# Kernel optimization log

Hardware: AMD Instinct MI355X
Metric: run time of the kernel (lower is better)

Reference implementation:

```python
import jax, jax.numpy as jnp
import numpy as np

IN_CH = 256
INTER_CH = IN_CH // 2  # reduction=2


def setup_inputs() -> dict:
    key = jax.random.key(0)
    ks = jax.random.split(key, 9)
    x = jax.random.normal(ks[0], (8, IN_CH, 64, 64), dtype=jnp.float32)
    std = 0.01
    # 1x1 conv weights stored as [out_ch, in_ch] (kernel is 1x1)
    Wg = jax.random.normal(ks[1], (INTER_CH, IN_CH), dtype=jnp.float32) * std
    bg = jnp.zeros((INTER_CH,), dtype=jnp.float32)
    Wt = jax.random.normal(ks[2], (INTER_CH, IN_CH), dtype=jnp.float32) * std
    bt = jnp.zeros((INTER_CH,), dtype=jnp.float32)
    Wp = jax.random.normal(ks[3], (INTER_CH, IN_CH), dtype=jnp.float32) * std
    bp = jnp.zeros((INTER_CH,), dtype=jnp.float32)
    # conv_out is zero-initialized in the module; use small random values so
    Wo = jax.random.normal(ks[4], (IN_CH, INTER_CH), dtype=jnp.float32) * std
    bo = jnp.zeros((IN_CH,), dtype=jnp.float32)
    return {"x": x, "Wg": Wg, "bg": bg, "Wt": Wt, "bt": bt,
            "Wp": Wp, "bp": bp, "Wo": Wo, "bo": bo}


def reference(x, Wg, bg, Wt, bt, Wp, bp, Wo, bo):
    n, c, h, w = x.shape
    s = h * w
    xf = x.reshape(n, c, s)  # [n, C, S]
    # 1x1 conv projections (no downsample, embedded_gaussian mode)
    g_x = jnp.einsum('kc,ncs->nsk', Wg, xf) + bg          # [n, S, K]
    theta_x = jnp.einsum('kc,ncs->nsk', Wt, xf) + bt      # [n, S, K]
    phi_x = jnp.einsum('kc,ncs->nks', Wp, xf) + bp[:, None]  # [n, K, S]
    # embedded_gaussian: scores -> scale (fixbug: / sqrt(K)) -> /temp(=1) -> softmax
    scale = 1.0 / jnp.sqrt(jnp.asarray(INTER_CH, dtype=x.dtype))
    scores = jnp.einsum('nsk,nkt->nst', theta_x, phi_x) * scale  # [n, S, S]
    pw = jax.nn.softmax(scores, axis=-1)
    y = jnp.einsum('nst,ntk->nsk', pw, g_x)               # [n, S, K]
    out = xf + jnp.einsum('ck,nsk->ncs', Wo, y) + bo[None, :, None]
    return out.reshape(n, c, h, w)
```

## Files before the change

kernel.cpp:

```cpp
#include <hip/hip_runtime.h>
#include <hip/hip_bf16.h>

#define NB   8
#define CCH  256
#define KCH  128
#define SSP  4096

typedef unsigned short u16;
typedef __attribute__((ext_vector_type(8))) short  bfrag;
typedef __attribute__((ext_vector_type(4))) float  ffrag;

#define MFMA16(a, b, c) __builtin_amdgcn_mfma_f32_16x16x32_bf16((a), (b), (c), 0, 0, 0)
#define SWZ(i, r) ((unsigned)(i) ^ ((((unsigned)(r)) & 7u) << 3))

#define GLDS(G, L) __builtin_amdgcn_global_load_lds(                          \
    (const __attribute__((address_space(1))) void*)(G),                       \
    (__attribute__((address_space(3))) void*)(L), 16, 0, 0)

__device__ __forceinline__ u16 f2b(float f) {
    union { float f; unsigned u; } v; v.f = f;
    return (u16)((v.u + 0x7fffu + ((v.u >> 16) & 1u)) >> 16);
}

__global__ __launch_bounds__(256, 2) void proj_gp_kernel(
    const float* __restrict__ x,
    const float* __restrict__ Wg, const float* __restrict__ bg,
    const float* __restrict__ Wp, const float* __restrict__ bp,
    u16* __restrict__ G,
    u16* __restrict__ P)
{
    __shared__ __align__(16) u16 sm[25600];
    const int tid  = threadIdx.x;
    const int wv   = tid >> 6;
    const int lane = tid & 63;
    const int quad = lane >> 4, l16 = lane & 15;
    const int bid  = blockIdx.x;
    const int n  = bid & 7;
    const int s0 = (bid >> 3) * 64;

    const ffrag zf = {0.f, 0.f, 0.f, 0.f};
    ffrag ga[8], pa[8];
#pragma unroll
    for (int kb = 0; kb < 8; kb++) { ga[kb] = zf; pa[kb] = zf; }

    float4 xreg[2], wgreg[4], wpreg[4];

#define K1_LOAD(C0)                                                          \
    {                                                                        \
        _Pragma("unroll")                                                    \
        for (int i = 0; i < 2; i++) {                                        \
            int f = tid + i * 256;                                           \
            int c = f >> 4, s4 = (f & 15) * 4;                               \
            xreg[i] = *(const float4*)&x[((size_t)n * CCH + (C0) + c) * SSP + s0 + s4]; \
        }                                                                    \
        _Pragma("unroll")                                                    \
        for (int i = 0; i < 4; i++) {                                        \
            int f = tid + i * 256;                                           \
            int k = f >> 3, co = (f & 7) * 4;                                \
            wgreg[i] = *(const float4*)&Wg[k * CCH + (C0) + co];             \
            wpreg[i] = *(const float4*)&Wp[k * CCH + (C0) + co];             \
        }                                                                    \
    }

#define K1_COMMIT(B)                                                         \
    {                                                                        \
        const int bb = (B) * 12800;                                          \
        _Pragma("unroll")                                                    \
        for (int i = 0; i < 2; i++) {                                        \
            int f = tid + i * 256;                                           \
            int c = f >> 4, s4 = (f & 15) * 4;                               \
            sm[bb + (s4 + 0) * 40 + c] = f2b(xreg[i].x);                     \
            sm[bb + (s4 + 1) * 40 + c] = f2b(xreg[i].y);                     \
            sm[bb + (s4 + 2) * 40 + c] = f2b(xreg[i].z);                     \
            sm[bb + (s4 + 3) * 40 + c] = f2b(xreg[i].w);                     \
        }                                                                    \
        _Pragma("unroll")                                                    \
        for (int i = 0; i < 4; i++) {                                        \
            int f = tid + i * 256;                                           \
            int k = f >> 3, co = (f & 7) * 4;                                \
            ushort4 g4 = {f2b(wgreg[i].x), f2b(wgreg[i].y), f2b(wgreg[i].z), f2b(wgreg[i].w)}; \
            ushort4 p4 = {f2b(wpreg[i].x), f2b(wpreg[i].y), f2b(wpreg[i].z), f2b(wpreg[i].w)}; \
            *(ushort4*)&sm[bb + 2560 + k * 40 + co] = g4;                    \
            *(ushort4*)&sm[bb + 7680 + k * 40 + co] = p4;                    \
        }                                                                    \
    }

    K1_LOAD(0)
    K1_COMMIT(0)
    K1_LOAD(32)
    asm volatile("s_waitcnt lgkmcnt(0)" ::: "memory");
    __builtin_amdgcn_s_barrier();

#pragma unroll
    for (int it = 0; it < 8; ++it) {
        if (it < 7) K1_COMMIT((it + 1) & 1)
        if (it < 6) K1_LOAD((it + 2) * 32)
        const int bb = (it & 1) * 12800;
        bfrag a = *(const bfrag*)&sm[bb + (16 * wv + l16) * 40 + quad * 8];
#pragma unroll
        for (int kb = 0; kb < 8; kb++) {
            bfrag bgf = *(const bfrag*)&sm[bb + 2560 + (16 * kb + l16) * 40 + quad * 8];
            bfrag bpf = *(const bfrag*)&sm[bb + 7680 + (16 * kb + l16) * 40 + quad * 8];
            ga[kb] = MFMA16(a, bgf, ga[kb]);
            pa[kb] = MFMA16(a, bpf, pa[kb]);
        }
        asm volatile("s_waitcnt lgkmcnt(0)" ::: "memory");
        __builtin_amdgcn_s_barrier();
    }
#undef K1_LOAD
#undef K1_COMMIT

#pragma unroll
    for (int kb = 0; kb < 8; kb++) {
        int k = l16 + 16 * kb;
        float bgv = bg[k], bpv = bp[k];
        int srow = s0 + 16 * wv + quad * 4;
        ushort4 g4 = {f2b(ga[kb][0] + bgv), f2b(ga[kb][1] + bgv),
                      f2b(ga[kb][2] + bgv), f2b(ga[kb][3] + bgv)};
        *(ushort4*)&G[(size_t)n * KCH * SSP + (size_t)k * SSP + srow] = g4;
#pragma unroll
        for (int r = 0; r < 4; r++)
            P[((size_t)n * SSP + srow + r) * KCH + k] = f2b(pa[kb][r] + bpv);
    }
}

__global__ __launch_bounds__(256, 2) void attn_fused_kernel(
    const float* __restrict__ x,
    const float* __restrict__ Wt, const float* __restrict__ bt,
    const u16* __restrict__ Pb,
    const u16* __restrict__ Gt,
    const float* __restrict__ Wo, const float* __restrict__ bo,
    float* __restrict__ out)
{
    __shared__ __align__(16) u16 sm[36864];
    const int tid  = threadIdx.x;
    const int wv   = tid >> 6;
    const int lane = tid & 63;
    const int quad = lane >> 4, l16 = lane & 15;
    const int wq   = wv & 1;
    const int tpar = wv >> 1;
    const int bid  = blockIdx.x;
    const int n    = bid & 7;
    const int q0   = (bid >> 3) * 64;
    const float qscale = 0.08838834764831845f * 1.4426950408889634f;
    const ffrag zf = {0.f, 0.f, 0.f, 0.f};

    const int KS0b = 0, KS1b = 8192, GT0b = 16384, GT1b = 24576, PSb = 32768;
    const int XTb = 8192, WTb = 10752, QSb = 8192;
    const int YSb = 24576, WOb = 16384;

    const u16* Pbase = Pb + (size_t)n * SSP * KCH;
    const u16* Gbase = Gt + (size_t)n * KCH * SSP;

#define STAGE_TILE(KSw, GTw, T0)                                             \
    {                                                                        \
        _Pragma("unroll")                                                    \
        for (int i = 0; i < 4; i++) {                                        \
            int chunk = wv * 4 + i;                                          \
            int row = chunk * 4 + (lane >> 4);                               \
            int cs  = ((lane & 15) * 8) ^ ((row & 7) << 3);                  \
            GLDS(Pbase + (size_t)((T0) + row) * KCH + cs,                    \
                 &sm[(KSw) + chunk * 512]);                                  \
        }                                                                    \
        _Pragma("unroll")                                                    \
        for (int i = 0; i < 4; i++) {                                        \
            int chunk = wv * 4 + i;                                          \
            int k  = chunk * 8 + (lane >> 3);                                \
            int cs = ((lane & 7) * 8) ^ ((k & 7) << 3);                      \
            GLDS(Gbase + (size_t)k * SSP + (T0) + cs,                        \
                 &sm[(GTw) + chunk * 512]);                                  \
        }                                                                    \
    }

    STAGE_TILE(KS0b, GT0b, 0)

    {
        ffrag qa[8];
#pragma unroll
        for (int kb = 0; kb < 8; kb++) qa[kb] = zf;

        for (int c0 = 0; c0 < CCH; c0 += 32) {
#pragma unroll
            for (int i = 0; i < 2; i++) {
                int f = tid + i * 256;
                int c = f >> 4, s4 = (f & 15) * 4;
                float4 xv = *(const float4*)&x[((size_t)n * CCH + c0 + c) * SSP + q0 + s4];
                sm[XTb + (s4 + 0) * 40 + c] = f2b(xv.x);
                sm[XTb + (s4 + 1) * 40 + c] = f2b(xv.y);
                sm[XTb + (s4 + 2) * 40 + c] = f2b(xv.z);
                sm[XTb + (s4 + 3) * 40 + c] = f2b(xv.w);
            }
#pragma unroll
            for (int i = 0; i < 4; i++) {
                int f = tid + i * 256;
                int k = f >> 3, co = (f & 7) * 4;
                float4 wq4 = *(const float4*)&Wt[k * CCH + c0 + co];
                ushort4 q4 = {f2b(wq4.x), f2b(wq4.y), f2b(wq4.z), f2b(wq4.w)};
                *(ushort4*)&sm[WTb + k * 40 + co] = q4;
            }
            __syncthreads();
            bfrag aq = *(const bfrag*)&sm[XTb + (16 * wv + l16) * 40 + quad * 8];
#pragma unroll
            for (int kb = 0; kb < 8; kb++) {
                bfrag bw = *(const bfrag*)&sm[WTb + (16 * kb + l16) * 40 + quad * 8];
                qa[kb] = MFMA16(aq, bw, qa[kb]);
            }
            __syncthreads();
        }
#pragma unroll
        for (int kb = 0; kb < 8; kb++) {
            float btv = bt[l16 + 16 * kb];
#pragma unroll
            for (int r = 0; r < 4; r++) {
                int row = 16 * wv + quad * 4 + r;
                sm[QSb + SWZ(row * 128 + l16 + 16 * kb, row)] = f2b((qa[kb][r] + btv) * qscale);
            }
        }
    }
    __syncthreads();

    bfrag qf[2][4];
#pragma unroll
    for (int qb = 0; qb < 2; qb++)
#pragma unroll
        for (int kc = 0; kc < 4; kc++)
            qf[qb][kc] = *(const bfrag*)&sm[QSb + SWZ((32 * wq + 16 * qb + l16) * 128 + kc * 32 + quad * 8, l16)];

    asm volatile("s_waitcnt vmcnt(0) lgkmcnt(0)" ::: "memory");
    __builtin_amdgcn_s_barrier();

    ffrag O[2][8];
#pragma unroll
    for (int qb = 0; qb < 2; qb++)
#pragma unroll
        for (int kb = 0; kb < 8; kb++) O[qb][kb] = zf;
    float l_r[2][4];
#pragma unroll
    for (int qb = 0; qb < 2; qb++)
#pragma unroll
        for (int r = 0; r < 4; r++) l_r[qb][r] = 0.f;

    const int NT = SSP / 64;
#pragma unroll 2
    for (int it = 0; it < NT; ++it) {
        const int cur = it & 1;
        const int KS  = cur ? KS1b : KS0b;
        const int GT  = cur ? GT1b : GT0b;

        if (it + 1 < NT) {
            const int KSw = cur ? KS0b : KS1b;
            const int GTw = cur ? GT0b : GT1b;
            STAGE_TILE(KSw, GTw, (it + 1) * 64)
        }

        ffrag sa[2][2];
#pragma unroll
        for (int qb = 0; qb < 2; qb++)
#pragma unroll
            for (int tb = 0; tb < 2; tb++) sa[qb][tb] = zf;
#pragma unroll
        for (int kc = 0; kc < 4; kc++)
#pragma unroll
            for (int tb = 0; tb < 2; tb++) {
                bfrag bk = *(const bfrag*)&sm[KS + SWZ((16 * (2 * tpar + tb) + l16) * 128 + kc * 32 + quad * 8, l16)];
                sa[0][tb] = MFMA16(qf[0][kc], bk, sa[0][tb]);
                sa[1][tb] = MFMA16(qf[1][kc], bk, sa[1][tb]);
            }

#pragma unroll
        for (int qb = 0; qb < 2; qb++)
#pragma unroll
            for (int r = 0; r < 4; r++) {
                float p0 = __builtin_amdgcn_exp2f(sa[qb][0][r]);
                float p1 = __builtin_amdgcn_exp2f(sa[qb][1][r]);
                l_r[qb][r] += p0 + p1;
                int row = 32 * wq + 16 * qb + quad * 4 + r;
                int cb0 = row * 64 + l16 + 32 * tpar;
                sm[PSb + SWZ(cb0,      row)] = f2b(p0);
                sm[PSb + SWZ(cb0 + 16, row)] = f2b(p1);
            }

        {
            bfrag ap0 = *(const bfrag*)&sm[PSb + SWZ((32 * wq + l16) * 64 + 32 * tpar + quad * 8, l16)];
            bfrag ap1 = *(const bfrag*)&sm[PSb + SWZ((32 * wq + 16 + l16) * 64 + 32 * tpar + quad * 8, l16)];
#pragma unroll
            for (int kb = 0; kb < 8; kb++) {
                bfrag bg = *(const bfrag*)&sm[GT + SWZ((16 * kb + l16) * 64 + 32 * tpar + quad * 8, l16)];
                O[0][kb] = MFMA16(ap0, bg, O[0][kb]);
                O[1][kb] = MFMA16(ap1, bg, O[1][kb]);
            }
        }

        asm volatile("s_waitcnt vmcnt(0) lgkmcnt(0)" ::: "memory");
        __builtin_amdgcn_s_barrier();
    }
#undef STAGE_TILE

#pragma unroll
    for (int qb = 0; qb < 2; qb++)
#pragma unroll
        for (int r = 0; r < 4; r++) {
            float rs = l_r[qb][r];
#pragma unroll
            for (int m = 1; m <= 8; m <<= 1) rs += __shfl_xor(rs, m);
            l_r[qb][r] = rs;
        }
    float* smf = (float*)sm;
    if (tpar == 1) {
#pragma unroll
        for (int qb = 0; qb < 2; qb++)
#pragma unroll
            for (int kb = 0; kb < 8; kb++)
#pragma unroll
                for (int r = 0; r < 4; r++) {
                    int row = 32 * wq + 16 * qb + quad * 4 + r;
                    smf[row * 128 + 16 * kb + l16] = O[qb][kb][r];
                }
        if (l16 == 0) {
#pragma unroll
            for (int qb = 0; qb < 2; qb++)
#pragma unroll
                for (int r = 0; r < 4; r++)
                    smf[16384 + 32 * wq + 16 * qb + quad * 4 + r] = l_r[qb][r];
        }
    }
    __syncthreads();
    if (tpar == 0) {
#pragma unroll
        for (int qb = 0; qb < 2; qb++)
#pragma unroll
            for (int r = 0; r < 4; r++) {
                int row = 32 * wq + 16 * qb + quad * 4 + r;
                float linv = 1.0f / (l_r[qb][r] + smf[16384 + row]);
#pragma unroll
                for (int kb = 0; kb < 8; kb++) {
                    int col = 16 * kb + l16;
                    float o = O[qb][kb][r] + smf[row * 128 + col];
                    sm[YSb + SWZ(row * 128 + col, row)] = f2b(o * linv);
                }
            }
    }

#pragma unroll
    for (int qtr = 0; qtr < 4; qtr++) {
        __syncthreads();
#pragma unroll
        for (int i = 0; i < 8; i++) {
            int f = tid + i * 256;
            int c = f >> 5, ko = (f & 31) * 4;
            float4 w = *(const float4*)&Wo[(size_t)(qtr * 64 + c) * KCH + ko];
            ushort4 w4 = {f2b(w.x), f2b(w.y), f2b(w.z), f2b(w.w)};
            *(ushort4*)&sm[WOb + SWZ(c * 128 + ko, c)] = w4;
        }
        __syncthreads();

        ffrag zc[4];
#pragma unroll
        for (int cb = 0; cb < 4; cb++) zc[cb] = zf;
#pragma unroll
        for (int kc = 0; kc < 4; kc++) {
            bfrag ay = *(const bfrag*)&sm[YSb + SWZ((16 * wv + l16) * 128 + kc * 32 + quad * 8, l16)];
#pragma unroll
            for (int cb = 0; cb < 4; cb++) {
                bfrag bw = *(const bfrag*)&sm[WOb + SWZ((16 * cb + l16) * 128 + kc * 32 + quad * 8, l16)];
                zc[cb] = MFMA16(ay, bw, zc[cb]);
            }
        }
#pragma unroll
        for (int cb = 0; cb < 4; cb++) {
            int c = qtr * 64 + 16 * cb + l16;
            float bc = bo[c];
            size_t base = ((size_t)n * CCH + c) * SSP + q0 + 16 * wv + quad * 4;
            float4 xv = *(const float4*)&x[base];
            float4 ov;
            ov.x = xv.x + zc[cb][0] + bc;
            ov.y = xv.y + zc[cb][1] + bc;
            ov.z = xv.z + zc[cb][2] + bc;
            ov.w = xv.w + zc[cb][3] + bc;
            *(float4*)&out[base] = ov;
        }
    }
}

extern "C" void kernel_launch(void* const* d_in, const int* in_sizes, int n_in,
                              void* d_out, int out_size, void* d_ws, size_t ws_size,
                              hipStream_t stream) {
    const float* x  = (const float*)d_in[0];
    const float* Wg = (const float*)d_in[1];
    const float* bg = (const float*)d_in[2];
    const float* Wt = (const float*)d_in[3];
    const float* bt = (const float*)d_in[4];
    const float* Wp = (const float*)d_in[5];
    const float* bp = (const float*)d_in[6];
    const float* Wo = (const float*)d_in[7];
    const float* bo = (const float*)d_in[8];
    float* out = (float*)d_out;

    u16* G = (u16*)d_ws;
    u16* P = G + (size_t)NB * SSP * KCH;

    proj_gp_kernel<<<dim3(NB * SSP / 64), 256, 0, stream>>>(x, Wg, bg, Wp, bp, G, P);
    attn_fused_kernel<<<dim3(NB * SSP / 64), 256, 0, stream>>>(x, Wt, bt, P, G, Wo, bo, out);
}
```

Before: 216.5 us.

## Load key and value fragments directly into registers instead of staging through LDS

The attention loop no longer double-buffers P/G tiles into shared memory with global_load_lds. Instead each wave owns 16 query rows and reads its key and value MFMA fragments straight from global memory into registers. The probability tile moves to a per-wave LDS slice, which removes the cross-wave split of the key dimension, the final O/l reduction through LDS, and the block barriers inside the loop. LDS use drops a lot, but each wave now fetches the whole K/G stream on its own, roughly quadrupling L2 traffic, and the loads are no longer prefetched ahead of use.

```diff
diff --git a/kernel.cpp b/kernel.cpp
--- a/kernel.cpp
+++ b/kernel.cpp
@@ -12,10 +12,6 @@
 
 #define MFMA16(a, b, c) __builtin_amdgcn_mfma_f32_16x16x32_bf16((a), (b), (c), 0, 0, 0)
 #define SWZ(i, r) ((unsigned)(i) ^ ((((unsigned)(r)) & 7u) << 3))
-
-#define GLDS(G, L) __builtin_amdgcn_global_load_lds(                          \
-    (const __attribute__((address_space(1))) void*)(G),                       \
-    (__attribute__((address_space(3))) void*)(L), 16, 0, 0)
 
 __device__ __forceinline__ u16 f2b(float f) {
     union { float f; unsigned u; } v; v.f = f;
@@ -132,47 +128,23 @@
     const float* __restrict__ Wo, const float* __restrict__ bo,
     float* __restrict__ out)
 {
-    __shared__ __align__(16) u16 sm[36864];
+    __shared__ __align__(16) u16 sm[16384];
     const int tid  = threadIdx.x;
     const int wv   = tid >> 6;
     const int lane = tid & 63;
     const int quad = lane >> 4, l16 = lane & 15;
-    const int wq   = wv & 1;
-    const int tpar = wv >> 1;
     const int bid  = blockIdx.x;
     const int n    = bid & 7;
     const int q0   = (bid >> 3) * 64;
     const float qscale = 0.08838834764831845f * 1.4426950408889634f;
     const ffrag zf = {0.f, 0.f, 0.f, 0.f};
 
-    const int KS0b = 0, KS1b = 8192, GT0b = 16384, GT1b = 24576, PSb = 32768;
-    const int XTb = 8192, WTb = 10752, QSb = 8192;
-    const int YSb = 24576, WOb = 16384;
+    const int QSb = 0, XTb = 8192, WTb = 10752;
+    const int PSw = 8192 + wv * 1024;
+    const int YSb = 0, WOb = 8192;
 
     const u16* Pbase = Pb + (size_t)n * SSP * KCH;
     const u16* Gbase = Gt + (size_t)n * KCH * SSP;
-
-#define STAGE_TILE(KSw, GTw, T0)                                             \
-    {                                                                        \
-        _Pragma("unroll")                                                    \
-        for (int i = 0; i < 4; i++) {                                        \
-            int chunk = wv * 4 + i;                                          \
-            int row = chunk * 4 + (lane >> 4);                               \
-            int cs  = ((lane & 15) * 8) ^ ((row & 7) << 3);                  \
-            GLDS(Pbase + (size_t)((T0) + row) * KCH + cs,                    \
-                 &sm[(KSw) + chunk * 512]);                                  \
-        }                                                                    \
-        _Pragma("unroll")                                                    \
-        for (int i = 0; i < 4; i++) {                                        \
-            int chunk = wv * 4 + i;                                          \
-            int k  = chunk * 8 + (lane >> 3);                                \
-            int cs = ((lane & 7) * 8) ^ ((k & 7) << 3);                      \
-            GLDS(Gbase + (size_t)k * SSP + (T0) + cs,                        \
-                 &sm[(GTw) + chunk * 512]);                                  \
-        }                                                                    \
-    }
-
-    STAGE_TILE(KS0b, GT0b, 0)
 
     {
         ffrag qa[8];
@@ -217,128 +189,85 @@
             }
         }
     }
-    __syncthreads();
-
-    bfrag qf[2][4];
-#pragma unroll
-    for (int qb = 0; qb < 2; qb++)
+
+    bfrag qf[4];
+#pragma unroll
+    for (int kc = 0; kc < 4; kc++)
+        qf[kc] = *(const bfrag*)&sm[QSb + SWZ((16 * wv + l16) * 128 + kc * 32 + quad * 8, l16)];
+
+    ffrag O[8];
+#pragma unroll
+    for (int kb = 0; kb < 8; kb++) O[kb] = zf;
+    float l_r[4] = {0.f, 0.f, 0.f, 0.f};
+
+    for (int t0 = 0; t0 < SSP; t0 += 64) {
+        bfrag kf[16];
+#pragma unroll
+        for (int tb = 0; tb < 4; tb++)
+#pragma unroll
+            for (int kc = 0; kc < 4; kc++)
+                kf[tb * 4 + kc] = *(const bfrag*)(Pbase
+                    + (size_t)(t0 + 16 * tb + l16) * KCH + kc * 32 + quad * 8);
+
+        ffrag sa[4];
+#pragma unroll
+        for (int tb = 0; tb < 4; tb++) sa[tb] = zf;
 #pragma unroll
         for (int kc = 0; kc < 4; kc++)
-            qf[qb][kc] = *(const bfrag*)&sm[QSb + SWZ((32 * wq + 16 * qb + l16) * 128 + kc * 32 + quad * 8, l16)];
-
-    asm volatile("s_waitcnt vmcnt(0) lgkmcnt(0)" ::: "memory");
-    __builtin_amdgcn_s_barrier();
-
-    ffrag O[2][8];
-#pragma unroll
-    for (int qb = 0; qb < 2; qb++)
-#pragma unroll
-        for (int kb = 0; kb < 8; kb++) O[qb][kb] = zf;
-    float l_r[2][4];
-#pragma unroll
-    for (int qb = 0; qb < 2; qb++)
-#pragma unroll
-        for (int r = 0; r < 4; r++) l_r[qb][r] = 0.f;
-
-    const int NT = SSP / 64;
-#pragma unroll 2
-    for (int it = 0; it < NT; ++it) {
-        const int cur = it & 1;
-        const int KS  = cur ? KS1b : KS0b;
-        const int GT  = cur ? GT1b : GT0b;
-
-        if (it + 1 < NT) {
-            const int KSw = cur ? KS0b : KS1b;
-            const int GTw = cur ? GT0b : GT1b;
-            STAGE_TILE(KSw, GTw, (it + 1) * 64)
-        }
-
-        ffrag sa[2][2];
-#pragma unroll
-        for (int qb = 0; qb < 2; qb++)
-#pragma unroll
-            for (int tb = 0; tb < 2; tb++) sa[qb][tb] = zf;
-#pragma unroll
-        for (int kc = 0; kc < 4; kc++)
-#pragma unroll
-            for (int tb = 0; tb < 2; tb++) {
-                bfrag bk = *(const bfrag*)&sm[KS + SWZ((16 * (2 * tpar + tb) + l16) * 128 + kc * 32 + quad * 8, l16)];
-                sa[0][tb] = MFMA16(qf[0][kc], bk, sa[0][tb]);
-                sa[1][tb] = MFMA16(qf[1][kc], bk, sa[1][tb]);
-            }
-
-#pragma unroll
-        for (int qb = 0; qb < 2; qb++)
-#pragma unroll
-            for (int r = 0; r < 4; r++) {
-                float p0 = __builtin_amdgcn_exp2f(sa[qb][0][r]);
-                float p1 = __builtin_amdgcn_exp2f(sa[qb][1][r]);
-                l_r[qb][r] += p0 + p1;
-                int row = 32 * wq + 16 * qb + quad * 4 + r;
-                int cb0 = row * 64 + l16 + 32 * tpar;
-                sm[PSb + SWZ(cb0,      row)] = f2b(p0);
-                sm[PSb + SWZ(cb0 + 16, row)] = f2b(p1);
-            }
-
-        {
-            bfrag ap0 = *(const bfrag*)&sm[PSb + SWZ((32 * wq + l16) * 64 + 32 * tpar + quad * 8, l16)];
-            bfrag ap1 = *(const bfrag*)&sm[PSb + SWZ((32 * wq + 16 + l16) * 64 + 32 * tpar + quad * 8, l16)];
-#pragma unroll
-            for (int kb = 0; kb < 8; kb++) {
-                bfrag bg = *(const bfrag*)&sm[GT + SWZ((16 * kb + l16) * 64 + 32 * tpar + quad * 8, l16)];
-                O[0][kb] = MFMA16(ap0, bg, O[0][kb]);
-                O[1][kb] = MFMA16(ap1, bg, O[1][kb]);
-            }
-        }
-
-        asm volatile("s_waitcnt vmcnt(0) lgkmcnt(0)" ::: "memory");
-        __builtin_amdgcn_s_barrier();
-    }
-#undef STAGE_TILE
-
-#pragma unroll
-    for (int qb = 0; qb < 2; qb++)
+#pragma unroll
+            for (int tb = 0; tb < 4; tb++)
+                sa[tb] = MFMA16(qf[kc], kf[tb * 4 + kc], sa[tb]);
+
+        bfrag gf[16];
+#pragma unroll
+        for (int kb = 0; kb < 8; kb++)
+#pragma unroll
+            for (int tc = 0; tc < 2; tc++)
+                gf[kb * 2 + tc] = *(const bfrag*)(Gbase
+                    + (size_t)(16 * kb + l16) * SSP + t0 + tc * 32 + quad * 8);
+
 #pragma unroll
         for (int r = 0; r < 4; r++) {
-            float rs = l_r[qb][r];
-#pragma unroll
-            for (int m = 1; m <= 8; m <<= 1) rs += __shfl_xor(rs, m);
-            l_r[qb][r] = rs;
-        }
-    float* smf = (float*)sm;
-    if (tpar == 1) {
-#pragma unroll
-        for (int qb = 0; qb < 2; qb++)
+            float p0 = __builtin_amdgcn_exp2f(sa[0][r]);
+            float p1 = __builtin_amdgcn_exp2f(sa[1][r]);
+            float p2 = __builtin_amdgcn_exp2f(sa[2][r]);
+            float p3 = __builtin_amdgcn_exp2f(sa[3][r]);
+            l_r[r] += (p0 + p1) + (p2 + p3);
+            int row = quad * 4 + r;
+            int rb = row * 64 + l16;
+            sm[PSw + SWZ(rb +  0, row)] = f2b(p0);
+            sm[PSw + SWZ(rb + 16, row)] = f2b(p1);
+            sm[PSw + SWZ(rb + 32, row)] = f2b(p2);
+            sm[PSw + SWZ(rb + 48, row)] = f2b(p3);
+        }
+
+#pragma unroll
+        for (int tc = 0; tc < 2; tc++) {
+            bfrag ap = *(const bfrag*)&sm[PSw + SWZ(l16 * 64 + tc * 32 + quad * 8, l16)];
 #pragma unroll
             for (int kb = 0; kb < 8; kb++)
-#pragma unroll
-                for (int r = 0; r < 4; r++) {
-                    int row = 32 * wq + 16 * qb + quad * 4 + r;
-                    smf[row * 128 + 16 * kb + l16] = O[qb][kb][r];
-                }
-        if (l16 == 0) {
-#pragma unroll
-            for (int qb = 0; qb < 2; qb++)
-#pragma unroll
-                for (int r = 0; r < 4; r++)
-                    smf[16384 + 32 * wq + 16 * qb + quad * 4 + r] = l_r[qb][r];
-        }
-    }
-    __syncthreads();
-    if (tpar == 0) {
-#pragma unroll
-        for (int qb = 0; qb < 2; qb++)
-#pragma unroll
-            for (int r = 0; r < 4; r++) {
-                int row = 32 * wq + 16 * qb + quad * 4 + r;
-                float linv = 1.0f / (l_r[qb][r] + smf[16384 + row]);
-#pragma unroll
-                for (int kb = 0; kb < 8; kb++) {
-                    int col = 16 * kb + l16;
-                    float o = O[qb][kb][r] + smf[row * 128 + col];
-                    sm[YSb + SWZ(row * 128 + col, row)] = f2b(o * linv);
-                }
-            }
+                O[kb] = MFMA16(ap, gf[kb * 2 + tc], O[kb]);
+        }
+    }
+
+    {
+        float rs0 = l_r[0], rs1 = l_r[1], rs2 = l_r[2], rs3 = l_r[3];
+#pragma unroll
+        for (int m = 1; m <= 8; m <<= 1) {
+            rs0 += __shfl_xor(rs0, m);
+            rs1 += __shfl_xor(rs1, m);
+            rs2 += __shfl_xor(rs2, m);
+            rs3 += __shfl_xor(rs3, m);
+        }
+        float lr0 = 1.0f / rs0, lr1 = 1.0f / rs1, lr2 = 1.0f / rs2, lr3 = 1.0f / rs3;
+#pragma unroll
+        for (int kb = 0; kb < 8; kb++) {
+            int rowb = 16 * wv + quad * 4;
+            sm[YSb + SWZ((rowb + 0) * 128 + l16 + 16 * kb, rowb + 0)] = f2b(O[kb][0] * lr0);
+            sm[YSb + SWZ((rowb + 1) * 128 + l16 + 16 * kb, rowb + 1)] = f2b(O[kb][1] * lr1);
+            sm[YSb + SWZ((rowb + 2) * 128 + l16 + 16 * kb, rowb + 2)] = f2b(O[kb][2] * lr2);
+            sm[YSb + SWZ((rowb + 3) * 128 + l16 + 16 * kb, rowb + 3)] = f2b(O[kb][3] * lr3);
+        }
     }
 
 #pragma unroll
```

Measured after the change: 574.4 us. 2.65x slower.
